# Performance work log

Measured on AMD Instinct MI355X. Metric: run time of the kernel, lower is better.

## Reference

```python
import jax, jax.numpy as jnp
import numpy as np

HEADS, DH, HID, EDGE_D = 8, 16, 128, 32  # heads, head_dim, hidden_dim, edge_dim
N, E = 50000, 800000


def _ln(x, w, b):
    mu = jnp.mean(x, axis=-1, keepdims=True)
    var = jnp.var(x, axis=-1, keepdims=True)
    return (x - mu) * jax.lax.rsqrt(var + 1e-5) * w + b


def setup_inputs() -> dict:
    key = jax.random.key(0)
    ks = jax.random.split(key, 16)
    lin = lambda k, fi, fo: (jax.random.normal(k, (fi, fo), jnp.float32) / np.sqrt(fi).astype(np.float32))
    inp = {
        'x': jax.random.normal(ks[0], (N, HID), jnp.float32),
        'edge_index': jax.random.randint(ks[1], (2, E), 0, N, jnp.int32),
        'edge_attr': jax.random.normal(ks[2], (E, EDGE_D), jnp.float32),
        'Wq': lin(ks[3], HID, HID), 'bq': jnp.zeros((HID,), jnp.float32),
        'Wk': lin(ks[4], HID, HID), 'bk': jnp.zeros((HID,), jnp.float32),
        'Wv': lin(ks[5], HID, HID), 'bv': jnp.zeros((HID,), jnp.float32),
        'We': lin(ks[6], EDGE_D, HID), 'be': jnp.zeros((HID,), jnp.float32),
        'Wskip': lin(ks[7], HID, HID), 'bskip': jnp.zeros((HID,), jnp.float32),
        'ln1_w': jnp.ones((HID,), jnp.float32), 'ln1_b': jnp.zeros((HID,), jnp.float32),
        'W1': lin(ks[8], HID, 4 * HID), 'b1': jnp.zeros((4 * HID,), jnp.float32),
        'W2': lin(ks[9], 4 * HID, HID), 'b2': jnp.zeros((HID,), jnp.float32),
        'ln2_w': jnp.ones((HID,), jnp.float32), 'ln2_b': jnp.zeros((HID,), jnp.float32),
    }
    return inp


def reference(x, edge_index, edge_attr, Wq, bq, Wk, bk, Wv, bv, We, be,
              Wskip, bskip, ln1_w, ln1_b, W1, b1, W2, b2, ln2_w, ln2_b):
    n = x.shape[0]
    src, dst = edge_index[0], edge_index[1]

    h = _ln(x, ln1_w, ln1_b)
    # projections, then per-edge gathers -> [E, H, Dh]
    q = (h @ Wq + bq)[dst].reshape(-1, HEADS, DH)
    k = (h @ Wk + bk)[src].reshape(-1, HEADS, DH)
    v = (h @ Wv + bv)[src].reshape(-1, HEADS, DH)
    e = (edge_attr @ We + be).reshape(-1, HEADS, DH)
    k = k + e
    v = v + e

    alpha = jnp.einsum('ehd,ehd->eh', q, k) / np.sqrt(DH).astype(np.float32)  # [E, H]
    # segment softmax over destination nodes (PyG softmax semantics)
    amax = jax.ops.segment_max(alpha, dst, num_segments=n)
    amax = jnp.where(jnp.isfinite(amax), amax, 0.0)
    expa = jnp.exp(alpha - amax[dst])
    denom = jax.ops.segment_sum(expa, dst, num_segments=n)
    alpha = expa / (denom[dst] + 1e-16)

    msg = jax.ops.segment_sum(alpha[..., None] * v, dst, num_segments=n)  # [N, H, Dh]
    conv_out = msg.reshape(n, HID) + h @ Wskip + bskip  # root_weight skip

    x = x + conv_out
    h2 = _ln(x, ln2_w, ln2_b)
    ffn = jax.nn.gelu(h2 @ W1 + b1, approximate=False) @ W2 + b2
    return x + ffn
```

## Files before the change

### kernel.cpp

```cpp
#include <hip/hip_runtime.h>
#include <math.h>

#define HID 128
#define EDGE_D 32
#define SC 0.36067376f
#define AS1 __attribute__((address_space(1)))
#define AS3 __attribute__((address_space(3)))

typedef unsigned short u16;
typedef unsigned int u32;
typedef __bf16 bf16x8 __attribute__((ext_vector_type(8)));
typedef float f32x4 __attribute__((ext_vector_type(4)));
typedef u32 u32x4 __attribute__((ext_vector_type(4)));
typedef u32 u32x2 __attribute__((ext_vector_type(2)));

static __device__ __forceinline__ u16 f2bf(float f) {
  u32 u = __float_as_uint(f);
  u += 0x7fffu + ((u >> 16) & 1u);
  return (u16)(u >> 16);
}
static __device__ __forceinline__ u32 pack2(float a, float b) {
  return (u32)f2bf(a) | ((u32)f2bf(b) << 16);
}
static __device__ __forceinline__ float bflo(u32 w) { return __uint_as_float(w << 16); }
static __device__ __forceinline__ float bfhi(u32 w) { return __uint_as_float(w & 0xffff0000u); }
static __device__ __forceinline__ float bf2f16(u16 b) {
  return __uint_as_float(((u32)b) << 16);
}
static __device__ __forceinline__ float grp16_sum(float x) {
  x += __int_as_float(__builtin_amdgcn_mov_dpp(__float_as_int(x), 0x128, 0xf, 0xf, true));
  x += __int_as_float(__builtin_amdgcn_mov_dpp(__float_as_int(x), 0x124, 0xf, 0xf, true));
  x += __int_as_float(__builtin_amdgcn_mov_dpp(__float_as_int(x), 0x122, 0xf, 0xf, true));
  x += __int_as_float(__builtin_amdgcn_mov_dpp(__float_as_int(x), 0x121, 0xf, 0xf, true));
  return x;
}
static __device__ __forceinline__ float wave_allreduce_sum(float v) {
#pragma unroll
  for (int off = 32; off > 0; off >>= 1) v += __shfl_xor(v, off);
  return v;
}

__global__ __launch_bounds__(256) void prelude_kernel(
    const float* __restrict__ Wq, const float* __restrict__ Wk,
    const float* __restrict__ Wv, const float* __restrict__ Ws,
    const float* __restrict__ W1, const float* __restrict__ W2,
    const float* __restrict__ We, const float* __restrict__ bq,
    u16* __restrict__ WqkvsT, u16* __restrict__ W1T, u16* __restrict__ W2T,
    u16* __restrict__ WbdT, u16* __restrict__ WfoldT, float* __restrict__ bfold,
    const float* __restrict__ x, u16* __restrict__ hout,
    const float* __restrict__ ln1w, const float* __restrict__ ln1b, int Nn,
    const int* __restrict__ dstp, int* __restrict__ cnt, int E) {
  int bid = blockIdx.x;
  if (bid < 1025) {
    int idx = bid * 256 + threadIdx.x;
    if (idx < 65536) {
      int m = idx >> 7, k = idx & 127;
      const float* Wm = m < 128 ? Wq : m < 256 ? Wk : m < 384 ? Wv : Ws;
      WqkvsT[idx] = f2bf(Wm[k * 128 + (m & 127)]);
    } else if (idx < 131072) {
      int j = idx - 65536;
      int m = j >> 7, k = j & 127;
      W1T[j] = f2bf(W1[k * 512 + m]);
    } else if (idx < 196608) {
      int j = idx - 131072;
      int m = j >> 9, k = j & 511;
      W2T[j] = f2bf(W2[k * 128 + m]);
    } else if (idx < 229376) {
      int j = idx - 196608;
      int m = j >> 8, c = j & 255;
      WbdT[j] = ((c >> 5) == (m >> 4)) ? f2bf(We[(c & 31) * 128 + m]) : (u16)0;
    } else if (idx < 262144) {
      int j = idx - 229376;
      int m = j >> 7, k = j & 127;
      int base = (m >> 5) * 16;
      const float* wq = Wq + k * 128 + base;
      const float* we = We + (m & 31) * 128 + base;
      float s = 0.f;
#pragma unroll
      for (int t = 0; t < 16; t++) s = fmaf(wq[t], we[t], s);
      WfoldT[j] = f2bf(s * SC);
    } else if (idx < 262400) {
      int m = idx - 262144;
      int base = (m >> 5) * 16;
      const float* we = We + (m & 31) * 128 + base;
      float s = 0.f;
#pragma unroll
      for (int t = 0; t < 16; t++) s = fmaf(bq[base + t], we[t], s);
      bfold[m] = s * SC;
    }
  } else if (bid < 2049) {
    int b = bid - 1025;
    int lane = threadIdx.x & 63;
    int row0 = b * 4 + (threadIdx.x >> 6);
    for (int row = row0; row < Nn; row += 4096) {
      const float* p = x + (size_t)row * HID;
      float a = p[lane], c = p[lane + 64];
      float s = wave_allreduce_sum(a + c);
      float s2 = wave_allreduce_sum(a * a + c * c);
      float mean = s * (1.f / 128.f);
      float var = s2 * (1.f / 128.f) - mean * mean;
      float rs = rsqrtf(var + 1e-5f);
      u16* o = hout + (size_t)row * HID;
      o[lane] = f2bf((a - mean) * rs * ln1w[lane] + ln1b[lane]);
      o[lane + 64] = f2bf((c - mean) * rs * ln1w[lane + 64] + ln1b[lane + 64]);
    }
  } else {
    int b = bid - 2049;
    for (int i = b * 256 + threadIdx.x; i < E; i += 262144)
      atomicAdd(&cnt[dstp[i]], 1);
  }
}

#define GSTAGE(buf, kc)                                                        \
  {                                                                            \
    _Pragma("unroll") for (int i = 0; i < 2; i++) {                            \
      int idx = i * 256 + t;                                                   \
      int row = idx >> 2, c4 = idx & 3;                                        \
      __builtin_amdgcn_global_load_lds(                                        \
          (const AS1 u32*)(A + (size_t)(r0 + row) * K + (kc) + c4 * 8),        \
          (AS3 u32*)&As[buf][idx * 8], 16, 0, 0);                              \
      __builtin_amdgcn_global_load_lds(                                        \
          (const AS1 u32*)(Bt + (size_t)(c0 + row) * K + (kc) + c4 * 8),       \
          (AS3 u32*)&Bs[buf][idx * 8], 16, 0, 0);                              \
    }                                                                          \
  }

#define GEMM_CORE                                                              \
  constexpr int NT = K / 32;                                                   \
  GSTAGE(0, 0)                                                                 \
  __syncthreads();                                                             \
  _Pragma("unroll") for (int tt = 0; tt < NT; tt++) {                          \
    if (tt + 1 < NT) GSTAGE((tt + 1) & 1, (tt + 1) * 32)                       \
    bf16x8 a0 = *(const bf16x8*)&As[tt & 1][(w * 32 + sr) * 32 + g * 8];       \
    bf16x8 a1 = *(const bf16x8*)&As[tt & 1][(w * 32 + 16 + sr) * 32 + g * 8];  \
    _Pragma("unroll") for (int nn = 0; nn < 8; nn++) {                         \
      bf16x8 b = *(const bf16x8*)&Bs[tt & 1][(nn * 16 + sr) * 32 + g * 8];     \
      acc[0][nn] = __builtin_amdgcn_mfma_f32_16x16x32_bf16(a0, b, acc[0][nn], 0, 0, 0); \
      acc[1][nn] = __builtin_amdgcn_mfma_f32_16x16x32_bf16(a1, b, acc[1][nn], 0, 0, 0); \
    }                                                                          \
    __syncthreads();                                                           \
  }

template <int K>
__global__ __launch_bounds__(256) void gemm_qkv(
    const u16* __restrict__ A, const u16* __restrict__ BtQ,
    const u16* __restrict__ BtF, int n,
    const float* __restrict__ bias0, const float* __restrict__ bias1,
    const float* __restrict__ bias2, const float* __restrict__ bfold,
    u32* __restrict__ opq, u32* __restrict__ pkv, u16* __restrict__ qweb16) {
  __shared__ u16 As[2][128 * 32];
  __shared__ u16 Bs[2][128 * 32];
  int t = threadIdx.x;
  int w = t >> 6, lane = t & 63;
  int g = lane >> 4, sr = lane & 15;
  int r0 = blockIdx.x * 128;
  int c0;
  const u16* Bt;
  if (blockIdx.y >= 3) {
    c0 = (blockIdx.y - 3) * 128;
    Bt = BtF;
  } else {
    c0 = blockIdx.y * 128;
    Bt = BtQ;
  }
  f32x4 acc[2][8];
#pragma unroll
  for (int m = 0; m < 2; m++)
#pragma unroll
    for (int nn = 0; nn < 8; nn++) acc[m][nn] = {0.f, 0.f, 0.f, 0.f};

  GEMM_CORE

  if (blockIdx.y == 0) {
#pragma unroll
    for (int m = 0; m < 2; m++)
#pragma unroll
      for (int nn = 0; nn < 4; nn++)
#pragma unroll
        for (int j = 0; j < 4; j++) {
          int row = r0 + w * 32 + m * 16 + g * 4 + j;
          if (row < n) {
            int cj = nn * 16 + sr;
            opq[((size_t)row << 6) + cj] =
                pack2(acc[m][nn][j] + bias0[cj], acc[m][nn + 4][j] + bias0[cj + 64]);
          }
        }
    return;
  }
  if (blockIdx.y < 3) {
    const float* bp = blockIdx.y == 1 ? bias1 : bias2;
    int which = blockIdx.y - 1;
#pragma unroll
    for (int m = 0; m < 2; m++)
#pragma unroll
      for (int nn = 0; nn < 4; nn++)
#pragma unroll
        for (int j = 0; j < 4; j++) {
          int row = r0 + w * 32 + m * 16 + g * 4 + j;
          if (row < n) {
            int cj = nn * 16 + sr;
            pkv[((size_t)row << 7) + (cj << 1) + which] =
                pack2(acc[m][nn][j] + bp[cj], acc[m][nn + 4][j] + bp[cj + 64]);
          }
        }
    return;
  }
  const float* bf = bfold + c0;
#pragma unroll
  for (int m = 0; m < 2; m++)
#pragma unroll
    for (int nn = 0; nn < 4; nn++)
#pragma unroll
      for (int j = 0; j < 4; j++) {
        int row = r0 + w * 32 + m * 16 + g * 4 + j;
        if (row < n) {
          int cj = nn * 16 + sr;
          u16* qrow = qweb16 + ((size_t)row << 8) + c0;
          qrow[cj] = f2bf(acc[m][nn][j] + bf[cj]);
          qrow[cj + 64] = f2bf(acc[m][nn + 4][j] + bf[cj + 64]);
        }
      }
}

__global__ __launch_bounds__(256) void gemm_bd_fin(
    const u16* __restrict__ Aw, const u16* __restrict__ BtW,
    const u16* __restrict__ Ah, const u16* __restrict__ BtS, int n,
    const float* __restrict__ x, const u32* __restrict__ msgb,
    const float* __restrict__ be, const float* __restrict__ bskip,
    const float* __restrict__ lnw, const float* __restrict__ lnb,
    u16* __restrict__ x1b, u16* __restrict__ h2) {
  __shared__ u16 As[2][128 * 32];
  __shared__ u16 Bs[2][128 * 32];
  int t = threadIdx.x;
  int w = t >> 6, lane = t & 63;
  int g = lane >> 4, sr = lane & 15;
  int r0 = blockIdx.x * 128;
  int c0 = 0;
  f32x4 acc[2][8];
#pragma unroll
  for (int m = 0; m < 2; m++)
#pragma unroll
    for (int nn = 0; nn < 8; nn++) acc[m][nn] = {0.f, 0.f, 0.f, 0.f};

  {
    const u16* A = Aw;
    const u16* Bt = BtW;
    constexpr int K = 256;
    GEMM_CORE
  }
  {
    const u16* A = Ah;
    const u16* Bt = BtS;
    constexpr int K = 128;
    GEMM_CORE
  }

  float becol[8], wcol[8], bcol[8], bscol[8];
#pragma unroll
  for (int nn = 0; nn < 8; nn++) {
    int c = nn * 16 + sr;
    becol[nn] = be[c];
    bscol[nn] = bskip[c];
    wcol[nn] = lnw[c];
    bcol[nn] = lnb[c];
  }
#pragma unroll
  for (int m = 0; m < 2; m++)
#pragma unroll
    for (int j = 0; j < 4; j++) {
      int row = r0 + w * 32 + m * 16 + g * 4 + j;
      if (row < n) {
        const float* xr = x + (size_t)row * HID;
        const u32* mr = msgb + ((size_t)row << 6);
        u16* x1r = x1b + (size_t)row * HID;
        u32 mw[4];
#pragma unroll
        for (int nn = 0; nn < 4; nn++) mw[nn] = mr[nn * 16 + sr];
        float tv[8];
        float s = 0.f, s2 = 0.f;
#pragma unroll
        for (int nn = 0; nn < 8; nn++) {
          int c = nn * 16 + sr;
          float mval = nn < 4 ? bflo(mw[nn]) : bfhi(mw[nn - 4]);
          float t1 = xr[c] + mval + acc[m][nn][j] + becol[nn] + bscol[nn];
          tv[nn] = t1;
          s += t1;
          s2 = fmaf(t1, t1, s2);
        }
        s = grp16_sum(s);
        s2 = grp16_sum(s2);
        float mean = s * (1.f / 128.f);
        float var = s2 * (1.f / 128.f) - mean * mean;
        float rs = rsqrtf(var + 1e-5f);
        u16* h2r = h2 + (size_t)row * HID;
#pragma unroll
        for (int nn = 0; nn < 8; nn++) {
          int c = nn * 16 + sr;
          x1r[c] = f2bf(tv[nn]);
          h2r[c] = f2bf((tv[nn] - mean) * rs * wcol[nn] + bcol[nn]);
        }
      }
    }
}

#define FSTAGE(buf, kc)                                                        \
  {                                                                            \
    {                                                                          \
      int row = t >> 2, c4 = t & 3;                                            \
      __builtin_amdgcn_global_load_lds(                                        \
          (const AS1 u32*)(h2 + (size_t)(r0 + row) * 128 + (kc) + c4 * 8),     \
          (AS3 u32*)&As[buf][t * 8], 16, 0, 0);                                \
    }                                                                          \
    _Pragma("unroll") for (int i = 0; i < 2; i++) {                            \
      int idx = i * 256 + t;                                                   \
      int row = idx >> 2, c4 = idx & 3;                                        \
      __builtin_amdgcn_global_load_lds(                                        \
          (const AS1 u32*)(W1T + (size_t)(c * 128 + row) * 128 + (kc) + c4 * 8), \
          (AS3 u32*)&Bs[buf][idx * 8], 16, 0, 0);                              \
    }                                                                          \
  }

__global__ __launch_bounds__(256) void ffn_fused(
    const u16* __restrict__ h2, const u16* __restrict__ W1T,
    const u16* __restrict__ W2T, const float* __restrict__ b1,
    const float* __restrict__ b2, const u16* __restrict__ x1b,
    float* __restrict__ out, int n) {
  __shared__ u16 As[2][64 * 32];
  __shared__ u16 Bs[2][128 * 32];
  __shared__ u16 T[64 * 136];
  __shared__ u16 Ws2[128 * 132];
  int t = threadIdx.x;
  int w = t >> 6, lane = t & 63;
  int g = lane >> 4, sr = lane & 15;
  int r0 = blockIdx.x * 64;
  f32x4 accO[8];
#pragma unroll
  for (int nn = 0; nn < 8; nn++) accO[nn] = {0.f, 0.f, 0.f, 0.f};

  for (int c = 0; c < 4; c++) {
#pragma unroll
    for (int i = 0; i < 8; i++) {
      int idx = i * 256 + t;
      int m = idx >> 4, k8 = idx & 15;
      u32x4 v = *(const u32x4*)(W2T + (size_t)m * 512 + c * 128 + k8 * 8);
      *(u32x4*)&Ws2[m * 132 + k8 * 8] = v;
    }
    f32x4 acc1[8];
#pragma unroll
    for (int nn = 0; nn < 8; nn++) acc1[nn] = {0.f, 0.f, 0.f, 0.f};
    FSTAGE(0, 0)
    __syncthreads();
#pragma unroll
    for (int tt = 0; tt < 4; tt++) {
      if (tt + 1 < 4) FSTAGE((tt + 1) & 1, (tt + 1) * 32)
      bf16x8 a = *(const bf16x8*)&As[tt & 1][(w * 16 + sr) * 32 + g * 8];
#pragma unroll
      for (int nn = 0; nn < 8; nn++) {
        bf16x8 b = *(const bf16x8*)&Bs[tt & 1][(nn * 16 + sr) * 32 + g * 8];
        acc1[nn] = __builtin_amdgcn_mfma_f32_16x16x32_bf16(a, b, acc1[nn], 0, 0, 0);
      }
      __syncthreads();
    }
#pragma unroll
    for (int nn = 0; nn < 8; nn++) {
      float bc = b1[c * 128 + nn * 16 + sr];
#pragma unroll
      for (int j = 0; j < 4; j++) {
        float v = acc1[nn][j] + bc;
        v = 0.5f * v * (1.f + erff(v * 0.70710678118f));
        T[(w * 16 + g * 4 + j) * 136 + nn * 16 + sr] = f2bf(v);
      }
    }
    __syncthreads();
#pragma unroll
    for (int tt = 0; tt < 4; tt++) {
      bf16x8 a = *(const bf16x8*)&T[(w * 16 + sr) * 136 + tt * 32 + g * 8];
#pragma unroll
      for (int nn = 0; nn < 8; nn++) {
        bf16x8 b = *(const bf16x8*)&Ws2[(nn * 16 + sr) * 132 + tt * 32 + g * 8];
        accO[nn] = __builtin_amdgcn_mfma_f32_16x16x32_bf16(a, b, accO[nn], 0, 0, 0);
      }
    }
    __syncthreads();
  }
#pragma unroll
  for (int nn = 0; nn < 8; nn++) {
#pragma unroll
    for (int j = 0; j < 4; j++) {
      int r = r0 + w * 16 + g * 4 + j;
      if (r < n) {
        int cj = nn * 16 + sr;
        out[(size_t)r * 128 + cj] =
            accO[nn][j] + b2[cj] + bf2f16(x1b[(size_t)r * 128 + cj]);
      }
    }
  }
}

__global__ __launch_bounds__(256) void scan_partial(const int* __restrict__ cnt,
                                                    int* __restrict__ bs, int N) {
  __shared__ int sd[256];
  int idx = blockIdx.x * 256 + threadIdx.x;
  sd[threadIdx.x] = (idx < N) ? cnt[idx] : 0;
  __syncthreads();
  for (int s = 128; s > 0; s >>= 1) {
    if (threadIdx.x < s) sd[threadIdx.x] += sd[threadIdx.x + s];
    __syncthreads();
  }
  if (threadIdx.x == 0) bs[blockIdx.x] = sd[0];
}

__global__ __launch_bounds__(256) void scan_final(const int* __restrict__ cnt,
                                                  const int* __restrict__ bs,
                                                  int* __restrict__ offs,
                                                  int* __restrict__ woff, int N,
                                                  int nb) {
  __shared__ int sb[256];
  __shared__ int sd[256];
  int t = threadIdx.x;
  sb[t] = (t < nb && t < (int)blockIdx.x) ? bs[t] : 0;
  __syncthreads();
  for (int s = 128; s > 0; s >>= 1) {
    if (t < s) sb[t] += sb[t + s];
    __syncthreads();
  }
  int base = sb[0];
  int idx = blockIdx.x * 256 + t;
  int v = (idx < N) ? cnt[idx] : 0;
  sd[t] = v;
  __syncthreads();
  for (int s = 1; s < 256; s <<= 1) {
    int add = (t >= s) ? sd[t - s] : 0;
    __syncthreads();
    sd[t] += add;
    __syncthreads();
  }
  if (idx < N) {
    int ex = sd[t] - v + base;
    offs[idx] = ex;
    woff[idx] = ex;
  }
}

__global__ __launch_bounds__(256) void scatter_kernel(const int* __restrict__ ei,
                                                      int* __restrict__ woff,
                                                      int2* __restrict__ sorted,
                                                      int E) {
  int i = blockIdx.x * blockDim.x + threadIdx.x;
  int stride = gridDim.x * blockDim.x;
  for (; i < E; i += stride) {
    int src = ei[i];
    int dst = ei[E + i];
    int pos = atomicAdd(&woff[dst], 1);
    sorted[pos] = make_int2(src, i);
  }
}

#define ISSUE4(P, base_)                                                       \
  {                                                                            \
    _Pragma("unroll") for (int jj = 0; jj < 4; jj++) {                         \
      int sj = min(base_ + jj, segn - 1);                                      \
      int sxx = __builtin_amdgcn_readlane(seRx, sj);                           \
      int syy = __builtin_amdgcn_readlane(seRy, sj);                           \
      P##kv[jj] = *(const u32x2*)(pkv + ((size_t)sxx << 7) + (lane << 1));     \
      P##ea[jj] = *(const float2*)(eaf + ((size_t)syy << 5) + 2 * sr);         \
    }                                                                          \
  }

#define COMP4(P, base_)                                                        \
  {                                                                            \
    _Pragma("unroll") for (int jj = 0; jj < 4; jj++) {                         \
      u32 kx = P##kv[jj].x, ky = P##kv[jj].y;                                  \
      float ex = P##ea[jj].x, ey = P##ea[jj].y;                                \
      float k0 = bflo(kx), k1 = bfhi(kx);                                      \
      float v0f = bflo(ky), v1f = bfhi(ky);                                    \
      float p0 = fmaf(q0C, k0, fmaf(qw0x, ex, qw0y * ey));                     \
      float p1 = fmaf(q1C, k1, fmaf(qw1x, ex, qw1y * ey));                     \
      p0 = grp16_sum(p0) + qb0C;                                               \
      p1 = grp16_sum(p1) + qb1C;                                               \
      bool val_ = (base_ + jj) < segn;                                         \
      float w1 = val_ ? __builtin_amdgcn_exp2f(p0) : 0.f;                      \
      float w2 = val_ ? __builtin_amdgcn_exp2f(p1) : 0.f;                      \
      l1 += w1;                                                                \
      l2 += w2;                                                                \
      a0 = fmaf(w1, v0f, a0);                                                  \
      a1 = fmaf(w2, v1f, a1);                                                  \
      wa00 = fmaf(w1, ex, wa00);                                               \
      wa01 = fmaf(w1, ey, wa01);                                               \
      wa10 = fmaf(w2, ex, wa10);                                               \
      wa11 = fmaf(w2, ey, wa11);                                               \
    }                                                                          \
  }

__global__ __launch_bounds__(256) void fused_edge(
    const int* __restrict__ offs, const int* __restrict__ cnt,
    const int2* __restrict__ sorted, const float* __restrict__ eaf,
    const float* __restrict__ be, const u32* __restrict__ pq,
    const u32* __restrict__ pkv, const u16* __restrict__ qweb16,
    u32* __restrict__ msgb, u32* __restrict__ weab, int Nn, int Etot) {
  int lane = threadIdx.x & 63;
  int w = threadIdx.x >> 6;
  int g = lane >> 4, sr = lane & 15;
  int wid = blockIdx.x * 4 + w;
  int nw = gridDim.x * 4;
  int per = (Nn + nw - 1) / nw;
  int n0 = wid * per;
  int n1 = min(Nn, n0 + per);
  if (n0 >= n1) return;
  int nn = n1 - n0;

  float be0 = be[lane], be1 = be[lane + 64];

  int ml = min(lane, nn - 1);
  int myBeg = offs[n0 + ml];
  int myCnt = cnt[n0 + ml];

  int beg = __builtin_amdgcn_readlane(myBeg, 0);
  int num = __builtin_amdgcn_readlane(myCnt, 0);
  int2 se2 = sorted[min(beg + min(lane, max(num - 1, 0)), Etot - 1)];
  int seCx = se2.x, seCy = se2.y;
  u32 pqC = pq[(size_t)n0 * 64 + lane];
  u32 qwb0C = *(const u32*)(qweb16 + ((size_t)n0 << 8) + g * 32 + 2 * sr);
  u32 qwb1C = *(const u32*)(qweb16 + ((size_t)n0 << 8) + (4 + g) * 32 + 2 * sr);

  for (int ni = 0; ni < nn; ni++) {
    int node = n0 + ni;
    int begX = 0, numX = 0, seXx = 0, seXy = 0;
    u32 pqX = 0, qwb0X = 0, qwb1X = 0;
    if (ni + 1 < nn) {
      begX = __builtin_amdgcn_readlane(myBeg, ni + 1);
      numX = __builtin_amdgcn_readlane(myCnt, ni + 1);
      int2 sx = sorted[min(begX + min(lane, max(numX - 1, 0)), Etot - 1)];
      seXx = sx.x;
      seXy = sx.y;
      pqX = pq[(size_t)(node + 1) * 64 + lane];
      qwb0X = *(const u32*)(qweb16 + ((size_t)(node + 1) << 8) + g * 32 + 2 * sr);
      qwb1X = *(const u32*)(qweb16 + ((size_t)(node + 1) << 8) + (4 + g) * 32 + 2 * sr);
    }
    float q0C = bflo(pqC) * SC, q1C = bfhi(pqC) * SC;
    float qw0x = bflo(qwb0C), qw0y = bfhi(qwb0C);
    float qw1x = bflo(qwb1C), qw1y = bfhi(qwb1C);
    float qb0C = grp16_sum(q0C * be0);
    float qb1C = grp16_sum(q1C * be1);
    float l1 = 0.f, l2 = 0.f, a0 = 0.f, a1 = 0.f;
    float wa00 = 0.f, wa01 = 0.f, wa10 = 0.f, wa11 = 0.f;
    if (num > 0) {
      int cb = 0;
      int seRx = seCx, seRy = seCy;
      while (true) {
        int segn = min(num - cb, 64);
        u32x2 Akv[4], Bkv[4];
        float2 Aea[4], Bea[4];
        ISSUE4(A, 0)
        for (int c = 0; c < segn; c += 8) {
          ISSUE4(B, c + 4)
          COMP4(A, c)
          ISSUE4(A, c + 8)
          COMP4(B, c + 4)
        }
        cb += 64;
        if (cb >= num) break;
        int rem = num - cb;
        int2 sn = sorted[min(beg + cb + min(lane, rem - 1), Etot - 1)];
        seRx = sn.x;
        seRy = sn.y;
      }
    }
    float inv1 = 1.f / (l1 + 1e-30f), inv2 = 1.f / (l2 + 1e-30f);
    if (num > 0) {
      msgb[((size_t)node << 6) + lane] = pack2(a0 * inv1, a1 * inv2);
    } else {
      msgb[((size_t)node << 6) + lane] = pack2(-be0, -be1);
    }
    weab[(size_t)node * 128 + g * 16 + sr] = pack2(wa00 * inv1, wa01 * inv1);
    weab[(size_t)node * 128 + 64 + g * 16 + sr] = pack2(wa10 * inv2, wa11 * inv2);
    beg = begX;
    num = numX;
    seCx = seXx;
    seCy = seXy;
    pqC = pqX;
    qwb0C = qwb0X;
    qwb1C = qwb1X;
  }
}

extern "C" void kernel_launch(void* const* d_in, const int* in_sizes, int n_in,
                              void* d_out, int out_size, void* d_ws, size_t ws_size,
                              hipStream_t stream) {
  const float* x = (const float*)d_in[0];
  const int* ei = (const int*)d_in[1];
  const float* ea = (const float*)d_in[2];
  const float* Wq = (const float*)d_in[3];
  const float* bq = (const float*)d_in[4];
  const float* Wk = (const float*)d_in[5];
  const float* bk = (const float*)d_in[6];
  const float* Wv = (const float*)d_in[7];
  const float* bv = (const float*)d_in[8];
  const float* We = (const float*)d_in[9];
  const float* be = (const float*)d_in[10];
  const float* Wskip = (const float*)d_in[11];
  const float* bskip = (const float*)d_in[12];
  const float* ln1w = (const float*)d_in[13];
  const float* ln1b = (const float*)d_in[14];
  const float* W1 = (const float*)d_in[15];
  const float* b1p = (const float*)d_in[16];
  const float* W2 = (const float*)d_in[17];
  const float* b2p = (const float*)d_in[18];
  const float* ln2w = (const float*)d_in[19];
  const float* ln2b = (const float*)d_in[20];

  int N = in_sizes[0] / HID;
  int E = in_sizes[1] / 2;
  size_t nf = (size_t)N * HID;

  float* ws = (float*)d_ws;
  size_t off = 0;
  u16* h_bf = (u16*)(ws + off); off += nf / 2;
  u32* pq = (u32*)(ws + off); off += nf / 2;
  u32* pkv = (u32*)(ws + off); off += nf;
  u16* x1b = (u16*)(ws + off); off += nf / 2;
  u32* msgb = (u32*)(ws + off); off += nf / 2;
  u32* weab = (u32*)(ws + off); off += nf;
  u16* qweb16 = (u16*)(ws + off); off += nf;
  int2* sorted = (int2*)(ws + off); off += (size_t)E * 2;
  int* cnt = (int*)(ws + off); off += N;
  int* offs = (int*)(ws + off); off += N;
  int* woff = (int*)(ws + off); off += N;
  int* bs = (int*)(ws + off); off += 256;
  u16* WqkvsT = (u16*)(ws + off); off += 32768;
  u16* W1T = (u16*)(ws + off); off += 32768;
  u16* W2T = (u16*)(ws + off); off += 32768;
  u16* WbdT = (u16*)(ws + off); off += 16384;
  u16* WfoldT = (u16*)(ws + off); off += 16384;
  float* bfold = ws + off; off += 256;
  u16* h2o = (u16*)pq;

  hipMemsetAsync(cnt, 0, (size_t)N * sizeof(int), stream);

  prelude_kernel<<<3073, 256, 0, stream>>>(Wq, Wk, Wv, Wskip, W1, W2, We, bq,
                                           WqkvsT, W1T, W2T, WbdT, WfoldT, bfold,
                                           x, h_bf, ln1w, ln1b, N, ei + E, cnt, E);

  dim3 gq((N + 127) / 128, 5);
  gemm_qkv<128><<<gq, 256, 0, stream>>>(h_bf, WqkvsT, WfoldT, N, bq, bk, bv,
                                        bfold, pq, pkv, qweb16);

  int nb = (N + 255) / 256;
  scan_partial<<<nb, 256, 0, stream>>>(cnt, bs, N);
  scan_final<<<nb, 256, 0, stream>>>(cnt, bs, offs, woff, N, nb);
  scatter_kernel<<<1024, 256, 0, stream>>>(ei, woff, sorted, E);

  int fe_blocks = (N + 15) / 16;
  fused_edge<<<fe_blocks, 256, 0, stream>>>(offs, cnt, sorted, ea, be, pq, pkv,
                                            qweb16, msgb, weab, N, E);

  dim3 ge((N + 127) / 128, 1);
  gemm_bd_fin<<<ge, 256, 0, stream>>>((const u16*)weab, WbdT, h_bf,
                                      WqkvsT + 384 * 128, N, x, msgb, be, bskip,
                                      ln2w, ln2b, x1b, h2o);

  ffn_fused<<<(N + 63) / 64, 256, 0, stream>>>(h2o, W1T, W2T, b1p, b2p, x1b,
                                               (float*)d_out, N);
}
```

Baseline: 362.5 us.

## Interleave edge processing of two destination nodes per wave for more memory parallelism

The per-node sequential loop in fused_edge becomes a fully unrolled scheme: each wave processes its nodes in pairs, and the gathers and online-softmax accumulation for both nodes of a pair are interleaved in one loop. This puts more independent K/V and edge_attr loads in flight, hiding gather latency across two nodes. The cost is a loop that runs to the larger of the two degrees, with masked wasted work for the smaller one, and roughly double the live registers. The code now handles at most four nodes per wave, so it relies on the launch grid keeping nodes per wave at or below four.

```diff
diff --git a/kernel.cpp b/kernel.cpp
--- a/kernel.cpp
+++ b/kernel.cpp
@@ -6,6 +6,7 @@
 #define SC 0.36067376f
 #define AS1 __attribute__((address_space(1)))
 #define AS3 __attribute__((address_space(3)))
+#define RL __builtin_amdgcn_readlane
 
 typedef unsigned short u16;
 typedef unsigned int u32;
@@ -456,40 +457,110 @@
   }
 }
 
-#define ISSUE4(P, base_)                                                       \
+#define PAIR_ISSUE4(S, P, base_)                                               \
   {                                                                            \
     _Pragma("unroll") for (int jj = 0; jj < 4; jj++) {                         \
-      int sj = min(base_ + jj, segn - 1);                                      \
-      int sxx = __builtin_amdgcn_readlane(seRx, sj);                           \
-      int syy = __builtin_amdgcn_readlane(seRy, sj);                           \
-      P##kv[jj] = *(const u32x2*)(pkv + ((size_t)sxx << 7) + (lane << 1));     \
-      P##ea[jj] = *(const float2*)(eaf + ((size_t)syy << 5) + 2 * sr);         \
+      int sj = min((base_) + jj, sM1##S);                                      \
+      int sxx = RL(seRx##S, sj);                                               \
+      int syy = RL(seRy##S, sj);                                               \
+      kv##S##P[jj] = *(const u32x2*)(pkv + ((size_t)sxx << 7) + (lane << 1));  \
+      ea##S##P[jj] = *(const float2*)(eaf + ((size_t)syy << 5) + 2 * sr);      \
     }                                                                          \
   }
 
-#define COMP4(P, base_)                                                        \
+#define PAIR_COMP4(S, P, base_)                                                \
   {                                                                            \
     _Pragma("unroll") for (int jj = 0; jj < 4; jj++) {                         \
-      u32 kx = P##kv[jj].x, ky = P##kv[jj].y;                                  \
-      float ex = P##ea[jj].x, ey = P##ea[jj].y;                                \
+      u32 kx = kv##S##P[jj].x, ky = kv##S##P[jj].y;                            \
+      float ex = ea##S##P[jj].x, ey = ea##S##P[jj].y;                          \
       float k0 = bflo(kx), k1 = bfhi(kx);                                      \
       float v0f = bflo(ky), v1f = bfhi(ky);                                    \
-      float p0 = fmaf(q0C, k0, fmaf(qw0x, ex, qw0y * ey));                     \
-      float p1 = fmaf(q1C, k1, fmaf(qw1x, ex, qw1y * ey));                     \
-      p0 = grp16_sum(p0) + qb0C;                                               \
-      p1 = grp16_sum(p1) + qb1C;                                               \
-      bool val_ = (base_ + jj) < segn;                                         \
+      float p0 = fmaf(q0C##S, k0, fmaf(qw0x##S, ex, qw0y##S * ey));            \
+      float p1 = fmaf(q1C##S, k1, fmaf(qw1x##S, ex, qw1y##S * ey));            \
+      p0 = grp16_sum(p0) + qb0C##S;                                            \
+      p1 = grp16_sum(p1) + qb1C##S;                                            \
+      bool val_ = (base_) + jj < segn##S;                                      \
       float w1 = val_ ? __builtin_amdgcn_exp2f(p0) : 0.f;                      \
       float w2 = val_ ? __builtin_amdgcn_exp2f(p1) : 0.f;                      \
-      l1 += w1;                                                                \
-      l2 += w2;                                                                \
-      a0 = fmaf(w1, v0f, a0);                                                  \
-      a1 = fmaf(w2, v1f, a1);                                                  \
-      wa00 = fmaf(w1, ex, wa00);                                               \
-      wa01 = fmaf(w1, ey, wa01);                                               \
-      wa10 = fmaf(w2, ex, wa10);                                               \
-      wa11 = fmaf(w2, ey, wa11);                                               \
+      l1##S += w1;                                                             \
+      l2##S += w2;                                                             \
+      a0##S = fmaf(w1, v0f, a0##S);                                            \
+      a1##S = fmaf(w2, v1f, a1##S);                                            \
+      wa00##S = fmaf(w1, ex, wa00##S);                                         \
+      wa01##S = fmaf(w1, ey, wa01##S);                                         \
+      wa10##S = fmaf(w2, ex, wa10##S);                                         \
+      wa11##S = fmaf(w2, ey, wa11##S);                                         \
     }                                                                          \
+  }
+
+#define EPILOGUE(S, node_, num_)                                               \
+  {                                                                            \
+    float inv1 = 1.f / (l1##S + 1e-30f), inv2 = 1.f / (l2##S + 1e-30f);        \
+    if ((num_) > 0)                                                            \
+      msgb[((size_t)(node_) << 6) + lane] = pack2(a0##S * inv1, a1##S * inv2); \
+    else                                                                       \
+      msgb[((size_t)(node_) << 6) + lane] = pack2(-be0, -be1);                 \
+    weab[(size_t)(node_)*128 + g * 16 + sr] = pack2(wa00##S * inv1, wa01##S * inv1); \
+    weab[(size_t)(node_)*128 + 64 + g * 16 + sr] = pack2(wa10##S * inv2, wa11##S * inv2); \
+  }
+
+#define RUN_PAIR(nodeA_, begA_, numA_, seA_, pqA_, qwA0_, qwA1_, nodeB_, begB_, \
+                 numB_, seB_, pqB_, qwB0_, qwB1_, exB_)                        \
+  {                                                                            \
+    float q0CA = bflo(pqA_) * SC, q1CA = bfhi(pqA_) * SC;                      \
+    float qw0xA = bflo(qwA0_), qw0yA = bfhi(qwA0_);                            \
+    float qw1xA = bflo(qwA1_), qw1yA = bfhi(qwA1_);                            \
+    float qb0CA = grp16_sum(q0CA * be0);                                       \
+    float qb1CA = grp16_sum(q1CA * be1);                                       \
+    float q0CB = bflo(pqB_) * SC, q1CB = bfhi(pqB_) * SC;                      \
+    float qw0xB = bflo(qwB0_), qw0yB = bfhi(qwB0_);                            \
+    float qw1xB = bflo(qwB1_), qw1yB = bfhi(qwB1_);                            \
+    float qb0CB = grp16_sum(q0CB * be0);                                       \
+    float qb1CB = grp16_sum(q1CB * be1);                                       \
+    float l1A = 0.f, l2A = 0.f, a0A = 0.f, a1A = 0.f;                          \
+    float wa00A = 0.f, wa01A = 0.f, wa10A = 0.f, wa11A = 0.f;                  \
+    float l1B = 0.f, l2B = 0.f, a0B = 0.f, a1B = 0.f;                          \
+    float wa00B = 0.f, wa01B = 0.f, wa10B = 0.f, wa11B = 0.f;                  \
+    int seRxA = (seA_).x, seRyA = (seA_).y;                                    \
+    int seRxB = (seB_).x, seRyB = (seB_).y;                                    \
+    int cbA = 0, cbB = 0;                                                      \
+    u32x2 kvA0[4], kvA1[4], kvB0[4], kvB1[4];                                  \
+    float2 eaA0[4], eaA1[4], eaB0[4], eaB1[4];                                 \
+    while (cbA < (numA_) || cbB < (numB_)) {                                   \
+      int segnA = max(min((numA_)-cbA, 64), 0);                                \
+      int segnB = max(min((numB_)-cbB, 64), 0);                                \
+      int sM1A = max(segnA - 1, 0);                                            \
+      int sM1B = max(segnB - 1, 0);                                            \
+      PAIR_ISSUE4(A, 0, 0)                                                     \
+      PAIR_ISSUE4(B, 0, 0)                                                     \
+      int maxn = max(segnA, segnB);                                            \
+      for (int c = 0; c < maxn; c += 8) {                                      \
+        PAIR_ISSUE4(A, 1, c + 4)                                               \
+        PAIR_ISSUE4(B, 1, c + 4)                                               \
+        PAIR_COMP4(A, 0, c)                                                    \
+        PAIR_COMP4(B, 0, c)                                                    \
+        PAIR_ISSUE4(A, 0, c + 8)                                               \
+        PAIR_ISSUE4(B, 0, c + 8)                                               \
+        PAIR_COMP4(A, 1, c + 4)                                                \
+        PAIR_COMP4(B, 1, c + 4)                                                \
+      }                                                                        \
+      cbA += 64;                                                               \
+      cbB += 64;                                                               \
+      if (cbA < (numA_)) {                                                     \
+        int rem = (numA_)-cbA;                                                 \
+        int2 sx = sorted[min((begA_) + cbA + min(lane, rem - 1), Etot - 1)];   \
+        seRxA = sx.x;                                                          \
+        seRyA = sx.y;                                                          \
+      }                                                                        \
+      if (cbB < (numB_)) {                                                     \
+        int rem = (numB_)-cbB;                                                 \
+        int2 sx = sorted[min((begB_) + cbB + min(lane, rem - 1), Etot - 1)];   \
+        seRxB = sx.x;                                                          \
+        seRyB = sx.y;                                                          \
+      }                                                                        \
+    }                                                                          \
+    EPILOGUE(A, nodeA_, numA_)                                                 \
+    if (exB_) EPILOGUE(B, nodeB_, numB_)                                       \
   }
 
 __global__ __launch_bounds__(256) void fused_edge(
@@ -515,72 +586,35 @@
   int myBeg = offs[n0 + ml];
   int myCnt = cnt[n0 + ml];
 
-  int beg = __builtin_amdgcn_readlane(myBeg, 0);
-  int num = __builtin_amdgcn_readlane(myCnt, 0);
-  int2 se2 = sorted[min(beg + min(lane, max(num - 1, 0)), Etot - 1)];
-  int seCx = se2.x, seCy = se2.y;
-  u32 pqC = pq[(size_t)n0 * 64 + lane];
-  u32 qwb0C = *(const u32*)(qweb16 + ((size_t)n0 << 8) + g * 32 + 2 * sr);
-  u32 qwb1C = *(const u32*)(qweb16 + ((size_t)n0 << 8) + (4 + g) * 32 + 2 * sr);
-
-  for (int ni = 0; ni < nn; ni++) {
-    int node = n0 + ni;
-    int begX = 0, numX = 0, seXx = 0, seXy = 0;
-    u32 pqX = 0, qwb0X = 0, qwb1X = 0;
-    if (ni + 1 < nn) {
-      begX = __builtin_amdgcn_readlane(myBeg, ni + 1);
-      numX = __builtin_amdgcn_readlane(myCnt, ni + 1);
-      int2 sx = sorted[min(begX + min(lane, max(numX - 1, 0)), Etot - 1)];
-      seXx = sx.x;
-      seXy = sx.y;
-      pqX = pq[(size_t)(node + 1) * 64 + lane];
-      qwb0X = *(const u32*)(qweb16 + ((size_t)(node + 1) << 8) + g * 32 + 2 * sr);
-      qwb1X = *(const u32*)(qweb16 + ((size_t)(node + 1) << 8) + (4 + g) * 32 + 2 * sr);
-    }
-    float q0C = bflo(pqC) * SC, q1C = bfhi(pqC) * SC;
-    float qw0x = bflo(qwb0C), qw0y = bfhi(qwb0C);
-    float qw1x = bflo(qwb1C), qw1y = bfhi(qwb1C);
-    float qb0C = grp16_sum(q0C * be0);
-    float qb1C = grp16_sum(q1C * be1);
-    float l1 = 0.f, l2 = 0.f, a0 = 0.f, a1 = 0.f;
-    float wa00 = 0.f, wa01 = 0.f, wa10 = 0.f, wa11 = 0.f;
-    if (num > 0) {
-      int cb = 0;
-      int seRx = seCx, seRy = seCy;
-      while (true) {
-        int segn = min(num - cb, 64);
-        u32x2 Akv[4], Bkv[4];
-        float2 Aea[4], Bea[4];
-        ISSUE4(A, 0)
-        for (int c = 0; c < segn; c += 8) {
-          ISSUE4(B, c + 4)
-          COMP4(A, c)
-          ISSUE4(A, c + 8)
-          COMP4(B, c + 4)
-        }
-        cb += 64;
-        if (cb >= num) break;
-        int rem = num - cb;
-        int2 sn = sorted[min(beg + cb + min(lane, rem - 1), Etot - 1)];
-        seRx = sn.x;
-        seRy = sn.y;
-      }
-    }
-    float inv1 = 1.f / (l1 + 1e-30f), inv2 = 1.f / (l2 + 1e-30f);
-    if (num > 0) {
-      msgb[((size_t)node << 6) + lane] = pack2(a0 * inv1, a1 * inv2);
-    } else {
-      msgb[((size_t)node << 6) + lane] = pack2(-be0, -be1);
-    }
-    weab[(size_t)node * 128 + g * 16 + sr] = pack2(wa00 * inv1, wa01 * inv1);
-    weab[(size_t)node * 128 + 64 + g * 16 + sr] = pack2(wa10 * inv2, wa11 * inv2);
-    beg = begX;
-    num = numX;
-    seCx = seXx;
-    seCy = seXy;
-    pqC = pqX;
-    qwb0C = qwb0X;
-    qwb1C = qwb1X;
+  int beg0 = RL(myBeg, 0), num0 = RL(myCnt, 0);
+  int beg1 = 0, num1 = 0, beg2 = 0, num2 = 0, beg3 = 0, num3 = 0;
+  if (nn > 1) { beg1 = RL(myBeg, 1); num1 = RL(myCnt, 1); }
+  if (nn > 2) { beg2 = RL(myBeg, 2); num2 = RL(myCnt, 2); }
+  if (nn > 3) { beg3 = RL(myBeg, 3); num3 = RL(myCnt, 3); }
+
+  int nd1 = n0 + min(1, nn - 1), nd2 = n0 + min(2, nn - 1), nd3 = n0 + min(3, nn - 1);
+  int2 se0 = sorted[min(beg0 + min(lane, max(num0 - 1, 0)), Etot - 1)];
+  int2 se1 = sorted[min(beg1 + min(lane, max(num1 - 1, 0)), Etot - 1)];
+  int2 se2 = sorted[min(beg2 + min(lane, max(num2 - 1, 0)), Etot - 1)];
+  int2 se3 = sorted[min(beg3 + min(lane, max(num3 - 1, 0)), Etot - 1)];
+  u32 pq0 = pq[(size_t)n0 * 64 + lane];
+  u32 pq1 = pq[(size_t)nd1 * 64 + lane];
+  u32 pq2 = pq[(size_t)nd2 * 64 + lane];
+  u32 pq3 = pq[(size_t)nd3 * 64 + lane];
+  u32 qa0 = *(const u32*)(qweb16 + ((size_t)n0 << 8) + g * 32 + 2 * sr);
+  u32 qb0_ = *(const u32*)(qweb16 + ((size_t)n0 << 8) + (4 + g) * 32 + 2 * sr);
+  u32 qa1 = *(const u32*)(qweb16 + ((size_t)nd1 << 8) + g * 32 + 2 * sr);
+  u32 qb1_ = *(const u32*)(qweb16 + ((size_t)nd1 << 8) + (4 + g) * 32 + 2 * sr);
+  u32 qa2 = *(const u32*)(qweb16 + ((size_t)nd2 << 8) + g * 32 + 2 * sr);
+  u32 qb2_ = *(const u32*)(qweb16 + ((size_t)nd2 << 8) + (4 + g) * 32 + 2 * sr);
+  u32 qa3 = *(const u32*)(qweb16 + ((size_t)nd3 << 8) + g * 32 + 2 * sr);
+  u32 qb3_ = *(const u32*)(qweb16 + ((size_t)nd3 << 8) + (4 + g) * 32 + 2 * sr);
+
+  RUN_PAIR(n0, beg0, num0, se0, pq0, qa0, qb0_, n0 + 1, beg1, num1, se1, pq1,
+           qa1, qb1_, (nn > 1))
+  if (nn > 2) {
+    RUN_PAIR(n0 + 2, beg2, num2, se2, pq2, qa2, qb2_, n0 + 3, beg3, num3, se3,
+             pq3, qa3, qb3_, (nn > 3))
   }
 }
 
```

After: 405.3 us. 1.12x slower.
